# Performance work log

Hardware: AMD Instinct MI355X
Metric: run time of the kernel (lower is better)

The kernel has to match this reference:

```python
import jax, jax.numpy as jnp
import numpy as np

K = 4        # num_kernels
TOPK = 16    # per-row hyperedge sparsification
CHEB_T = 2   # Chebyshev order
ROW_TEMP = 1.0
PI_ITERS = 5  # power-iteration steps


def setup_inputs() -> dict:
    key = jax.random.key(0)
    N, D, D_out = 4096, 256, 256
    ks = jax.random.split(key, 5)
    X = jax.random.normal(ks[0], (N, D), jnp.float32)
    L_k = jax.random.normal(ks[1], (K, D, D), jnp.float32) * 0.02
    alpha = jnp.ones((K,), jnp.float32)
    theta = jax.random.normal(ks[2], (CHEB_T + 1, D), jnp.float32) * 0.02
    rho_raw = jnp.zeros((), jnp.float32)
    proj_w = jax.random.normal(ks[3], (D_out, D), jnp.float32) / np.sqrt(D).astype(np.float32)
    proj_b = jnp.zeros((D_out,), jnp.float32)
    return {"X": X, "L_k": L_k, "alpha": alpha, "theta": theta,
            "rho_raw": rho_raw, "proj_w": proj_w, "proj_b": proj_b}


def reference(X, L_k, alpha, theta, rho_raw, proj_w, proj_b):
    N, D = X.shape
    tau = max(ROW_TEMP, 1e-6)
    # 1) K bilinear kernels: A_k = X L_k X^T / sqrt(D), row-softmax with temp
    A = jnp.einsum('nd,kde,me->knm', X, L_k, X) / jnp.sqrt(jnp.asarray(D, X.dtype))
    H_stack = jax.nn.softmax(A / tau, axis=2)                 # (K, N, N)
    w = jax.nn.softmax(alpha)[:, None, None]
    H_fused = (H_stack * w).sum(0)                            # (N, N)
    # 2) incidence B (N, E=K*N): hyperedge (k,i) holds topk targets of row i of head k
    vals, idx = jax.lax.top_k(H_stack, TOPK)                  # (K, N, TOPK)
    vals = vals / (vals.sum(-1, keepdims=True) + 1e-9)
    E = K * N
    cols = jnp.arange(K)[:, None, None] * N + jnp.arange(N)[None, :, None]
    cols = jnp.broadcast_to(cols, (K, N, TOPK)).reshape(-1)
    rows = idx.reshape(-1)
    B = jnp.zeros((N, E), X.dtype).at[rows, cols].set(vals.reshape(-1))
    W = jnp.ones((E,), X.dtype)
    # 3) normalized hypergraph Laplacian L = I - Dv^{-1/2} B W De^{-1} B^T Dv^{-1/2}
    De = B.sum(0) + 1e-9                                      # (E,)
    Dv = (B * W[None, :]).sum(1) + 1e-9                       # (N,)
    Dv_is = jnp.sqrt(1.0 / Dv)
    S = (B * (W / De)[None, :]) @ B.T                         # (N, N)
    S_norm = Dv_is[:, None] * S * Dv_is[None, :]
    I = jnp.eye(N, dtype=X.dtype)
    L = I - S_norm
    # 4) lambda_max via power iteration on detached L (constant w.r.t. grads)
    Ld = jax.lax.stop_gradient(L)
    v = jax.random.normal(jax.random.key(1), (N, 1), X.dtype)
    v = v / (jnp.linalg.norm(v) + 1e-9)
    for _ in range(PI_ITERS):
        v = Ld @ v
        v = v / (jnp.linalg.norm(v) + 1e-9)
    lam = jnp.clip((v.T @ (Ld @ v)).squeeze(), 1e-3, None)
    lam = jax.lax.stop_gradient(lam)
    L_tilde = (2.0 / lam) * L - I
    # Chebyshev recursion: sum_t T_t(L_tilde) X * theta_t, then ELU
    T0 = X
    out = T0 * theta[0][None, :]
    T1 = L_tilde @ X
    out = out + T1 * theta[1][None, :]
    for t in range(2, CHEB_T + 1):
        T2 = 2.0 * (L_tilde @ T1) - T0
        out = out + T2 * theta[t][None, :]
        T0, T1 = T1, T2
    Z_spec = jax.nn.elu(out)
    # 5) residual blend with kernel diffusion
    Z_kern = H_fused @ X
    rho = jax.nn.sigmoid(rho_raw)
    Z_mix = rho * Z_spec + (1.0 - rho) * Z_kern
    # 6) final projection
    return Z_mix @ proj_w.T + proj_b
```

## Files before the change

### kernel.cpp

```cpp
#include <hip/hip_runtime.h>

typedef unsigned short u16;
typedef unsigned long long u64;
typedef _Float16 h16;
typedef __attribute__((ext_vector_type(8))) _Float16 h16x8;
typedef __attribute__((ext_vector_type(4))) _Float16 h16x4;
typedef __attribute__((ext_vector_type(4))) float f32x4;

__device__ __forceinline__ float b2f(u16 u) {
  unsigned x = ((unsigned)u) << 16;
  return __uint_as_float(x);
}
__device__ __forceinline__ unsigned fkey(float f) {
  unsigned b = __float_as_uint(f);
  return (b & 0x80000000u) ? ~b : (b | 0x80000000u);
}
__device__ __forceinline__ float unfkey(unsigned u) {
  unsigned b = (u & 0x80000000u) ? (u ^ 0x80000000u) : ~u;
  return __uint_as_float(b);
}
__device__ __forceinline__ f32x4 mfma16(h16x8 a, h16x8 b, f32x4 c) {
  return __builtin_amdgcn_mfma_f32_16x16x32_f16(a, b, c, 0, 0, 0);
}
__device__ __forceinline__ void gl_lds16(const void* g, void* l) {
  __builtin_amdgcn_global_load_lds(
      (const __attribute__((address_space(1))) unsigned*)g,
      (__attribute__((address_space(3))) unsigned*)l, 16, 0, 0);
}
__device__ __forceinline__ u64 wave_max_u64(u64 k) {
#pragma unroll
  for (int off = 32; off; off >>= 1) {
    u64 o = __shfl_xor(k, off);
    if (o > k) k = o;
  }
  return k;
}

__global__ void detect_dtype(const u16* __restrict__ X, int* __restrict__ flag) {
  __shared__ int cnt;
  if (threadIdx.x == 0) cnt = 0;
  __syncthreads();
  int sane = 0;
#pragma unroll
  for (int j = 0; j < 16; ++j) {
    u16 u = X[(threadIdx.x * 16 + j) * 2];
    int e = (u >> 7) & 0xff;
    if (u == 0 || (e >= 112 && e <= 142)) sane++;
  }
  atomicAdd(&cnt, sane);
  __syncthreads();
  if (threadIdx.x == 0) *flag = (cnt < 3072) ? 1 : 0;
}

__global__ __launch_bounds__(256) void split_input3(
    const void* __restrict__ in, h16* __restrict__ hi, h16* __restrict__ lo,
    float* __restrict__ f32out, int n, const int* __restrict__ flag) {
  int f = *flag;
  int stride = gridDim.x * 256;
  for (int i = blockIdx.x * 256 + threadIdx.x; i < n; i += stride) {
    float x = f ? ((const float*)in)[i] : b2f(((const u16*)in)[i]);
    h16 h = (h16)x;
    hi[i] = h;
    lo[i] = (h16)(x - (float)h);
    if (f32out) f32out[i] = x;
  }
}

__global__ __launch_bounds__(256) void split_f32h(
    const float* __restrict__ in, h16* __restrict__ hi, h16* __restrict__ lo,
    int n) {
  int stride = gridDim.x * 256;
  for (int i = blockIdx.x * 256 + threadIdx.x; i < n; i += stride) {
    float x = in[i];
    h16 h = (h16)x;
    hi[i] = h;
    lo[i] = (h16)(x - (float)h);
  }
}

__global__ __launch_bounds__(256) void conv_f32(const void* __restrict__ in,
                                                float* __restrict__ out, int n,
                                                const int* __restrict__ flag) {
  int f = *flag;
  int stride = gridDim.x * 256;
  for (int i = blockIdx.x * 256 + threadIdx.x; i < n; i += stride)
    out[i] = f ? ((const float*)in)[i] : b2f(((const u16*)in)[i]);
}

template <bool BIAS>
__global__ __launch_bounds__(256) void gemm3_nt(
    const h16* __restrict__ Ah, const h16* __restrict__ Al,
    const h16* __restrict__ Bh, const h16* __restrict__ Bl,
    float* __restrict__ C, const float* __restrict__ bias, float alpha,
    int M, int Nc, int Kd, long batchA, long batchB, long batchC) {
  const h16* Abh = Ah + (size_t)blockIdx.z * batchA;
  const h16* Abl = Al + (size_t)blockIdx.z * batchA;
  const h16* Bbh = Bh + (size_t)blockIdx.z * batchB;
  const h16* Bbl = Bl + (size_t)blockIdx.z * batchB;
  float* Cb = C + (size_t)blockIdx.z * batchC;
  int bn = blockIdx.x, bm = blockIdx.y;
  int tid = threadIdx.x;
  int wid = tid >> 6, lane = tid & 63;
  __shared__ h16 Ash[64 * 40], Asl[64 * 40], Bsh[64 * 40], Bsl[64 * 40];
  f32x4 acc00 = {}, acc01 = {}, acc10 = {}, acc11 = {};
  int lr = tid >> 2;
  int lc = (tid & 3) << 3;
  size_t aoff = (size_t)(bm * 64 + lr) * Kd + lc;
  size_t boff = (size_t)(bn * 64 + lr) * Kd + lc;
  int wm = (wid & 1) * 32, wn = (wid >> 1) * 32;
  int fr = lane & 15;
  int fc = (lane >> 4) << 3;
  for (int k0 = 0; k0 < Kd; k0 += 32) {
    uint4 avh = *(const uint4*)(Abh + aoff + k0);
    uint4 avl = *(const uint4*)(Abl + aoff + k0);
    uint4 bvh = *(const uint4*)(Bbh + boff + k0);
    uint4 bvl = *(const uint4*)(Bbl + boff + k0);
    __syncthreads();
    *(uint4*)(Ash + lr * 40 + lc) = avh;
    *(uint4*)(Asl + lr * 40 + lc) = avl;
    *(uint4*)(Bsh + lr * 40 + lc) = bvh;
    *(uint4*)(Bsl + lr * 40 + lc) = bvl;
    __syncthreads();
    h16x8 a0h = *(const h16x8*)(Ash + (wm + fr) * 40 + fc);
    h16x8 a1h = *(const h16x8*)(Ash + (wm + 16 + fr) * 40 + fc);
    h16x8 b0h = *(const h16x8*)(Bsh + (wn + fr) * 40 + fc);
    h16x8 b1h = *(const h16x8*)(Bsh + (wn + 16 + fr) * 40 + fc);
    h16x8 a0l = *(const h16x8*)(Asl + (wm + fr) * 40 + fc);
    h16x8 a1l = *(const h16x8*)(Asl + (wm + 16 + fr) * 40 + fc);
    h16x8 b0l = *(const h16x8*)(Bsl + (wn + fr) * 40 + fc);
    h16x8 b1l = *(const h16x8*)(Bsl + (wn + 16 + fr) * 40 + fc);
    acc00 = mfma16(a0h, b0h, acc00);
    acc01 = mfma16(a0h, b1h, acc01);
    acc10 = mfma16(a1h, b0h, acc10);
    acc11 = mfma16(a1h, b1h, acc11);
    acc00 = mfma16(a0h, b0l, acc00);
    acc01 = mfma16(a0h, b1l, acc01);
    acc10 = mfma16(a1h, b0l, acc10);
    acc11 = mfma16(a1h, b1l, acc11);
    acc00 = mfma16(a0l, b0h, acc00);
    acc01 = mfma16(a0l, b1h, acc01);
    acc10 = mfma16(a1l, b0h, acc10);
    acc11 = mfma16(a1l, b1h, acc11);
  }
  int crow = (lane >> 4) << 2;
  int ccol = lane & 15;
  f32x4 accs[2][2] = {{acc00, acc01}, {acc10, acc11}};
#pragma unroll
  for (int i = 0; i < 2; ++i)
#pragma unroll
    for (int j = 0; j < 2; ++j) {
      int r0 = bm * 64 + wm + 16 * i + crow;
      int c0 = bn * 64 + wn + 16 * j + ccol;
#pragma unroll
      for (int rg = 0; rg < 4; ++rg) {
        float v = accs[i][j][rg] * alpha;
        if constexpr (BIAS) v += bias[c0];
        Cb[(size_t)(r0 + rg) * Nc + c0] = v;
      }
    }
}

__global__ __launch_bounds__(256) void gemm3_big(
    const h16* __restrict__ Ah, const h16* __restrict__ Al,
    const h16* __restrict__ Bh, const h16* __restrict__ Bl,
    float* __restrict__ C, float alpha, int M, int Nc, int Kd) {
  __shared__ h16 sAh[128 * 32], sAl[128 * 32], sBh[128 * 32], sBl[128 * 32];
  int tid = threadIdx.x, wid = tid >> 6, lane = tid & 63;
  int bm = blockIdx.y, bn = blockIdx.x;
  int srow = 32 * wid + (lane >> 2);
  int scnk = lane & 3;
  int fr = lane & 15, fcc = lane >> 4;
  f32x4 acc[4][4] = {};
  const h16* gA[2] = {Ah, Al};
  const h16* gB[2] = {Bh, Bl};
  h16* sA[2] = {sAh, sAl};
  h16* sB[2] = {sBh, sBl};
  int wm = (wid & 1) * 64, wn = (wid >> 1) * 64;
  for (int k0 = 0; k0 < Kd; k0 += 32) {
    __syncthreads();
#pragma unroll
    for (int h = 0; h < 2; ++h) {
      int r = srow + 16 * h;
      int cs = scnk ^ ((r >> 1) & 3);
      size_t goffA = (size_t)(bm * 128 + r) * Kd + k0 + cs * 8;
      size_t goffB = (size_t)(bn * 128 + r) * Kd + k0 + cs * 8;
      int loff = (32 * wid + 16 * h) * 32;
#pragma unroll
      for (int p = 0; p < 2; ++p) {
        gl_lds16(gA[p] + goffA, sA[p] + loff);
        gl_lds16(gB[p] + goffB, sB[p] + loff);
      }
    }
    __syncthreads();
    h16x8 fa[2][4], fb[2][4];
#pragma unroll
    for (int i = 0; i < 4; ++i) {
      int ra = wm + 16 * i + fr;
      int ca = (fcc ^ ((ra >> 1) & 3)) * 8;
      fa[0][i] = *(const h16x8*)(sAh + ra * 32 + ca);
      fa[1][i] = *(const h16x8*)(sAl + ra * 32 + ca);
      int rb = wn + 16 * i + fr;
      int cb = (fcc ^ ((rb >> 1) & 3)) * 8;
      fb[0][i] = *(const h16x8*)(sBh + rb * 32 + cb);
      fb[1][i] = *(const h16x8*)(sBl + rb * 32 + cb);
    }
#pragma unroll
    for (int i = 0; i < 4; ++i)
#pragma unroll
      for (int j = 0; j < 4; ++j) {
        acc[i][j] = mfma16(fa[0][i], fb[0][j], acc[i][j]);
        acc[i][j] = mfma16(fa[0][i], fb[1][j], acc[i][j]);
        acc[i][j] = mfma16(fa[1][i], fb[0][j], acc[i][j]);
      }
  }
  int crow = (lane >> 4) << 2, ccol = lane & 15;
#pragma unroll
  for (int i = 0; i < 4; ++i)
#pragma unroll
    for (int j = 0; j < 4; ++j) {
      int r0 = bm * 128 + wm + 16 * i + crow;
      int c0 = bn * 128 + wn + 16 * j + ccol;
#pragma unroll
      for (int rg = 0; rg < 4; ++rg)
        C[(size_t)(r0 + rg) * Nc + c0] = acc[i][j][rg] * alpha;
    }
}

__global__ __launch_bounds__(256) void gemm_ks(
    const h16* __restrict__ A, const h16* __restrict__ B,
    float* __restrict__ Cpart, int Kd, int Kc) {
  __shared__ h16 sA[128 * 32], sB[128 * 32];
  int tid = threadIdx.x, wid = tid >> 6, lane = tid & 63;
  int bm = blockIdx.y, bn = blockIdx.x, kz = blockIdx.z;
  int kbase = kz * Kc;
  int srow = 32 * wid + (lane >> 2);
  int scnk = lane & 3;
  int fr = lane & 15, fcc = lane >> 4;
  f32x4 acc[4][4] = {};
  int wm = (wid & 1) * 64, wn = (wid >> 1) * 64;
  for (int k0 = 0; k0 < Kc; k0 += 32) {
    __syncthreads();
#pragma unroll
    for (int h = 0; h < 2; ++h) {
      int r = srow + 16 * h;
      int cs = scnk ^ ((r >> 1) & 3);
      size_t goffA = (size_t)(bm * 128 + r) * Kd + kbase + k0 + cs * 8;
      size_t goffB = (size_t)(bn * 128 + r) * Kd + kbase + k0 + cs * 8;
      int loff = (32 * wid + 16 * h) * 32;
      gl_lds16(A + goffA, sA + loff);
      gl_lds16(B + goffB, sB + loff);
    }
    __syncthreads();
    h16x8 fa[4], fb[4];
#pragma unroll
    for (int i = 0; i < 4; ++i) {
      int ra = wm + 16 * i + fr;
      int ca = (fcc ^ ((ra >> 1) & 3)) * 8;
      fa[i] = *(const h16x8*)(sA + ra * 32 + ca);
      int rb = wn + 16 * i + fr;
      int cb = (fcc ^ ((rb >> 1) & 3)) * 8;
      fb[i] = *(const h16x8*)(sB + rb * 32 + cb);
    }
#pragma unroll
    for (int i = 0; i < 4; ++i)
#pragma unroll
      for (int j = 0; j < 4; ++j)
        acc[i][j] = mfma16(fa[i], fb[j], acc[i][j]);
  }
  float* Cp = Cpart + (size_t)kz * 4096 * 256;
  int crow = (lane >> 4) << 2, ccol = lane & 15;
#pragma unroll
  for (int i = 0; i < 4; ++i)
#pragma unroll
    for (int j = 0; j < 4; ++j) {
      int r0 = bm * 128 + wm + 16 * i + crow;
      int c0 = bn * 128 + wn + 16 * j + ccol;
#pragma unroll
      for (int rg = 0; rg < 4; ++rg)
        Cp[(size_t)(r0 + rg) * 256 + c0] = acc[i][j][rg];
    }
}

__global__ __launch_bounds__(256) void ks_reduce(
    const float* __restrict__ Cpart, const float* __restrict__ scptr,
    const float* __restrict__ rowSinv, float* __restrict__ Zk) {
  int i = (blockIdx.x * 256 + threadIdx.x) * 4;
  float4 s = {0.f, 0.f, 0.f, 0.f};
#pragma unroll
  for (int z = 0; z < 8; ++z) {
    float4 p = *(const float4*)(Cpart + (size_t)z * 4096 * 256 + i);
    s.x += p.x; s.y += p.y; s.z += p.z; s.w += p.w;
  }
  float sc = (*scptr) * rowSinv[i >> 8];
  float4 zk = *(float4*)(Zk + i);
  zk.x += sc * s.x; zk.y += sc * s.y; zk.z += sc * s.z; zk.w += sc * s.w;
  *(float4*)(Zk + i) = zk;
}

__global__ __launch_bounds__(256) void transpose16(
    const u16* __restrict__ in, u16* __restrict__ out, int rows, int cols) {
  __shared__ u16 t[32][33];
  const u16* ib = in + (size_t)blockIdx.z * rows * cols;
  u16* ob = out + (size_t)blockIdx.z * rows * cols;
  int r0 = blockIdx.x * 32, c0 = blockIdx.y * 32;
  int tx = threadIdx.x & 31, ty = threadIdx.x >> 5;
#pragma unroll
  for (int i = 0; i < 32; i += 8)
    t[ty + i][tx] = ib[(size_t)(r0 + ty + i) * cols + c0 + tx];
  __syncthreads();
#pragma unroll
  for (int i = 0; i < 32; i += 8)
    ob[(size_t)(c0 + ty + i) * rows + r0 + tx] = t[tx][ty + i];
}

__global__ void prep_scalars(const void* __restrict__ alpha,
                             const void* __restrict__ rho_raw,
                             float* __restrict__ scal,
                             const int* __restrict__ flag) {
  if (threadIdx.x == 0) {
    int f = *flag;
    float a[4], e[4], m = -1e30f, s = 0.f;
    for (int i = 0; i < 4; ++i) {
      a[i] = f ? ((const float*)alpha)[i] : b2f(((const u16*)alpha)[i]);
      m = fmaxf(m, a[i]);
    }
    for (int i = 0; i < 4; ++i) { e[i] = expf(a[i] - m); s += e[i]; }
    for (int i = 0; i < 4; ++i) scal[i] = e[i] / s;
    float rr = f ? ((const float*)rho_raw)[0] : b2f(((const u16*)rho_raw)[0]);
    scal[4] = 1.f / (1.f + expf(-rr));
  }
}

__global__ __launch_bounds__(256) void row_softmax_topk(
    const float* __restrict__ A, float* __restrict__ topv,
    int* __restrict__ topi, h16* __restrict__ E, float* __restrict__ rowSinv,
    int khead) {
  __shared__ u64 candK[4][256];
  __shared__ int candN[4];
  int wid = threadIdx.x >> 6, lane = threadIdx.x & 63;
  int row = blockIdx.x * 4 + wid;
  const float* arow = A + ((size_t)row << 12);
  if (lane == 0) candN[wid] = 0;
  __syncthreads();
  float lm = -INFINITY;
#pragma unroll
  for (int t = 0; t < 16; ++t) {
    float4 v = *(const float4*)(arow + (t << 8) + (lane << 2));
    lm = fmaxf(lm, fmaxf(fmaxf(v.x, v.y), fmaxf(v.z, v.w)));
  }
  float m = lm;
#pragma unroll
  for (int off = 32; off; off >>= 1) m = fmaxf(m, __shfl_xor(m, off));
  u64 lk = ((u64)fkey(lm) << 32) | (unsigned)lane;
  float T = 0.f;
  for (int r = 0; r < 16; ++r) {
    u64 k2 = wave_max_u64(lk);
    if (lk == k2) lk = 0;
    if (r == 15) T = unfkey((unsigned)(k2 >> 32));
  }
  h16* erow = E + ((size_t)row << 12);
  int* cn = &candN[wid];
  u64* ck = candK[wid];
  float s = 0.f;
  for (int t = 0; t < 16; ++t) {
    int c = (t << 8) + (lane << 2);
    float4 v = *(const float4*)(arow + c);
    float e0 = __expf(v.x - m), e1 = __expf(v.y - m);
    float e2 = __expf(v.z - m), e3 = __expf(v.w - m);
    s += (e0 + e1) + (e2 + e3);
    h16x4 hv = {(h16)e0, (h16)e1, (h16)e2, (h16)e3};
    *(h16x4*)(erow + c) = hv;
    if (v.x >= T) {
      int sl = atomicAdd(cn, 1);
      if (sl < 256) ck[sl] = ((u64)fkey(v.x) << 32) | (unsigned)(~(unsigned)c);
    }
    if (v.y >= T) {
      int sl = atomicAdd(cn, 1);
      if (sl < 256) ck[sl] = ((u64)fkey(v.y) << 32) | (unsigned)(~(unsigned)(c + 1));
    }
    if (v.z >= T) {
      int sl = atomicAdd(cn, 1);
      if (sl < 256) ck[sl] = ((u64)fkey(v.z) << 32) | (unsigned)(~(unsigned)(c + 2));
    }
    if (v.w >= T) {
      int sl = atomicAdd(cn, 1);
      if (sl < 256) ck[sl] = ((u64)fkey(v.w) << 32) | (unsigned)(~(unsigned)(c + 3));
    }
  }
#pragma unroll
  for (int off = 32; off; off >>= 1) s += __shfl_xor(s, off);
  if (lane == 0) rowSinv[row] = 1.f / s;
  __syncthreads();
  int cnt = min(*cn, 256);
  u64 loc[4] = {0ull, 0ull, 0ull, 0ull};
  int nl = 0;
  for (int j = lane; j < cnt; j += 64)
    if (nl < 4) loc[nl++] = ck[j];
#define CSW(a, b)                     \
  {                                   \
    if (loc[b] > loc[a]) {            \
      u64 tt = loc[a];                \
      loc[a] = loc[b];                \
      loc[b] = tt;                    \
    }                                 \
  }
  CSW(0, 1) CSW(2, 3) CSW(0, 2) CSW(1, 3) CSW(1, 2)
#undef CSW
  float myv = 0.f;
  int myi = 0;
  float sum16 = 0.f;
  for (int r = 0; r < 16; ++r) {
    u64 key = loc[0];
    u64 k2 = wave_max_u64(key);
    float wv = unfkey((unsigned)(k2 >> 32));
    int wi = (int)(~(unsigned)(k2 & 0xffffffffu));
    if (key == k2 && key != 0ull) {
      loc[0] = loc[1];
      loc[1] = loc[2];
      loc[2] = loc[3];
      loc[3] = 0ull;
    }
    sum16 += expf(wv - m);
    if (r == lane) { myv = wv; myi = wi; }
  }
  if (lane < 16) {
    size_t o = (((size_t)khead << 12) + row) * 16 + lane;
    topv[o] = expf(myv - m) / (sum16 + 1e-9f * s);
    topi[o] = myi;
  }
}

__global__ __launch_bounds__(256) void edge_prep2(
    const float* __restrict__ topv, const int* __restrict__ topi,
    float* __restrict__ Dv, int* __restrict__ cnt) {
  int t = blockIdx.x * 256 + threadIdx.x;
  float v = topv[t];
  int i = topi[t];
  atomicAdd(&Dv[i], v);
  atomicAdd(&cnt[i], 1);
}

__global__ __launch_bounds__(256) void edge_deis(
    const float* __restrict__ topv, float* __restrict__ DeIS) {
  int e = blockIdx.x * 256 + threadIdx.x;
  const float4* p = (const float4*)(topv + ((size_t)e << 4));
  float4 a = p[0], b = p[1], c = p[2], d = p[3];
  float s = ((a.x + a.y) + (a.z + a.w)) + ((b.x + b.y) + (b.z + b.w)) +
            ((c.x + c.y) + (c.z + c.w)) + ((d.x + d.y) + (d.z + d.w));
  DeIS[e] = 1.0f / sqrtf(s + 1e-9f);
}

__global__ void dv_isqrt(const float* __restrict__ Dv, float* __restrict__ Dvis) {
  int i = blockIdx.x * 256 + threadIdx.x;
  Dvis[i] = sqrtf(1.0f / (Dv[i] + 1e-9f));
}

__global__ __launch_bounds__(256) void scan_rowptr(const int* __restrict__ cnt,
                                                   int* __restrict__ rowptr,
                                                   int* __restrict__ cur) {
  __shared__ int part[256];
  int tid = threadIdx.x;
  int base = tid * 16;
  int loc[16];
  int s = 0;
#pragma unroll
  for (int j = 0; j < 16; ++j) { loc[j] = s; s += cnt[base + j]; }
  part[tid] = s;
  __syncthreads();
  for (int off = 1; off < 256; off <<= 1) {
    int v = (tid >= off) ? part[tid - off] : 0;
    __syncthreads();
    part[tid] += v;
    __syncthreads();
  }
  int pre = (tid == 0) ? 0 : part[tid - 1];
#pragma unroll
  for (int j = 0; j < 16; ++j) {
    int r = pre + loc[j];
    rowptr[base + j] = r;
    cur[base + j] = r;
  }
  if (tid == 255) rowptr[4096] = part[255];
}

__global__ __launch_bounds__(256) void csr_fill2(
    const float* __restrict__ topv, const int* __restrict__ topi,
    const float* __restrict__ Dvis, const float* __restrict__ DeIS,
    int* __restrict__ cur, float* __restrict__ cvals, int* __restrict__ colE,
    float* __restrict__ cvalR) {
  int t = blockIdx.x * 256 + threadIdx.x;
  int e = t >> 4;
  int i = topi[t];
  float c = Dvis[i] * topv[t] * DeIS[e];
  cvals[t] = c;
  int slot = atomicAdd(&cur[i], 1);
  colE[slot] = e;
  cvalR[slot] = c;
}

__global__ __launch_bounds__(256) void spmv_edge(
    const float* __restrict__ cvals, const int* __restrict__ topi,
    const float* __restrict__ v, float* __restrict__ g) {
  int e = blockIdx.x * 256 + threadIdx.x;
  float acc = 0.f;
#pragma unroll
  for (int p = 0; p < 16; ++p)
    acc += cvals[e * 16 + p] * v[topi[e * 16 + p]];
  g[e] = acc;
}

__global__ __launch_bounds__(256) void spmv_row(
    const int* __restrict__ rowptr, const int* __restrict__ colE,
    const float* __restrict__ cvalR, const float* __restrict__ g,
    const float* __restrict__ vin, float* __restrict__ vout) {
  int wid = threadIdx.x >> 6, lane = threadIdx.x & 63;
  int row = blockIdx.x * 4 + wid;
  int s = rowptr[row], e = rowptr[row + 1];
  float acc = 0.f;
  for (int j = s + lane; j < e; j += 64) acc += cvalR[j] * g[colE[j]];
#pragma unroll
  for (int off = 32; off; off >>= 1) acc += __shfl_xor(acc, off);
  if (lane == 0) vout[row] = vin[row] - acc;
}

__global__ __launch_bounds__(256) void spmm_edge(
    const float* __restrict__ cvals, const int* __restrict__ topi,
    const float* __restrict__ M, float* __restrict__ G) {
  int wid = threadIdx.x >> 6, lane = threadIdx.x & 63;
  int e = blockIdx.x * 4 + wid;
  int cb = lane << 2;
  const float* cv = cvals + ((size_t)e << 4);
  const int* ti = topi + ((size_t)e << 4);
  float cc[16];
  int ix[16];
#pragma unroll
  for (int p = 0; p < 16; ++p) { cc[p] = cv[p]; ix[p] = ti[p]; }
  float4 acc[4] = {};
#pragma unroll
  for (int h = 0; h < 2; ++h) {
    float4 g[8];
#pragma unroll
    for (int p = 0; p < 8; ++p)
      g[p] = *(const float4*)(M + ((size_t)ix[h * 8 + p] << 8) + cb);
#pragma unroll
    for (int p = 0; p < 8; ++p) {
      float c = cc[h * 8 + p];
      float4 gg = g[p];
      int a = p & 3;
      acc[a].x += c * gg.x; acc[a].y += c * gg.y;
      acc[a].z += c * gg.z; acc[a].w += c * gg.w;
    }
  }
  float4 r;
  r.x = (acc[0].x + acc[1].x) + (acc[2].x + acc[3].x);
  r.y = (acc[0].y + acc[1].y) + (acc[2].y + acc[3].y);
  r.z = (acc[0].z + acc[1].z) + (acc[2].z + acc[3].z);
  r.w = (acc[0].w + acc[1].w) + (acc[2].w + acc[3].w);
  *(float4*)(G + ((size_t)e << 8) + cb) = r;
}

__global__ __launch_bounds__(256) void spmm_row(
    const int* __restrict__ rowptr, const int* __restrict__ colE,
    const float* __restrict__ cvalR, const float* __restrict__ G,
    float* __restrict__ Z) {
  int wid = threadIdx.x >> 6, lane = threadIdx.x & 63;
  int row = blockIdx.x * 4 + wid;
  int cb = lane << 2;
  int s = rowptr[row], e = rowptr[row + 1];
  float4 acc[4] = {};
  int j = s;
  for (; j + 8 <= e; j += 8) {
    int ix[8];
    float cc[8];
#pragma unroll
    for (int t = 0; t < 8; ++t) { ix[t] = colE[j + t]; cc[t] = cvalR[j + t]; }
    float4 g[8];
#pragma unroll
    for (int t = 0; t < 8; ++t)
      g[t] = *(const float4*)(G + ((size_t)ix[t] << 8) + cb);
#pragma unroll
    for (int t = 0; t < 8; ++t) {
      float c = cc[t];
      float4 gg = g[t];
      int a = t & 3;
      acc[a].x += c * gg.x; acc[a].y += c * gg.y;
      acc[a].z += c * gg.z; acc[a].w += c * gg.w;
    }
  }
  for (; j < e; ++j) {
    float c = cvalR[j];
    float4 gg = *(const float4*)(G + ((size_t)colE[j] << 8) + cb);
    acc[0].x += c * gg.x; acc[0].y += c * gg.y;
    acc[0].z += c * gg.z; acc[0].w += c * gg.w;
  }
  float4 r;
  r.x = (acc[0].x + acc[1].x) + (acc[2].x + acc[3].x);
  r.y = (acc[0].y + acc[1].y) + (acc[2].y + acc[3].y);
  r.z = (acc[0].z + acc[1].z) + (acc[2].z + acc[3].z);
  r.w = (acc[0].w + acc[1].w) + (acc[2].w + acc[3].w);
  *(float4*)(Z + ((size_t)row << 8) + cb) = r;
}

__global__ __launch_bounds__(256) void init_v0(float* __restrict__ v) {
  int tid = blockIdx.x * 256 + threadIdx.x;
  unsigned j = (unsigned)(tid & 2047);
  unsigned x0 = j, x1 = j + 2048u;
  const unsigned ks0 = 0u, ks1 = 1u, ks2 = 0x1BD11BDAu;
  x0 += ks0; x1 += ks1;
#define TF_R(r)                                  \
  {                                              \
    x0 += x1;                                    \
    x1 = (x1 << (r)) | (x1 >> (32 - (r)));       \
    x1 ^= x0;                                    \
  }
  TF_R(13) TF_R(15) TF_R(26) TF_R(6)  x0 += ks1; x1 += ks2 + 1u;
  TF_R(17) TF_R(29) TF_R(16) TF_R(24) x0 += ks2; x1 += ks0 + 2u;
  TF_R(13) TF_R(15) TF_R(26) TF_R(6)  x0 += ks0; x1 += ks1 + 3u;
  TF_R(17) TF_R(29) TF_R(16) TF_R(24) x0 += ks1; x1 += ks2 + 4u;
  TF_R(13) TF_R(15) TF_R(26) TF_R(6)  x0 += ks2; x1 += ks0 + 5u;
#undef TF_R
  unsigned bits = (tid < 2048) ? x0 : x1;
  float u01 = __uint_as_float((bits >> 9) | 0x3f800000u) - 1.0f;
  const float lo = -0.99999994f;
  float u = fmaxf(lo, u01 * 2.0f + lo);
  float w = -log1pf(-u * u);
  float p;
  if (w < 5.0f) {
    float t = w - 2.5f;
    p = 2.81022636e-08f;
    p = 3.43273939e-07f + p * t;
    p = -3.5233877e-06f + p * t;
    p = -4.39150654e-06f + p * t;
    p = 0.00021858087f + p * t;
    p = -0.00125372503f + p * t;
    p = -0.00417768164f + p * t;
    p = 0.246640727f + p * t;
    p = 1.50140941f + p * t;
  } else {
    float t = sqrtf(w) - 3.0f;
    p = -0.000200214257f;
    p = 0.000100950558f + p * t;
    p = 0.00134934322f + p * t;
    p = -0.00367342844f + p * t;
    p = 0.00573950773f + p * t;
    p = -0.0076224613f + p * t;
    p = 0.00943887047f + p * t;
    p = 1.00167406f + p * t;
    p = 2.83297682f + p * t;
  }
  v[tid] = 1.41421354f * (p * u);
}

__global__ __launch_bounds__(256) void pi_dots(const float* __restrict__ w5,
                                               const float* __restrict__ w6,
                                               float* __restrict__ scal) {
  __shared__ float r1[256], r2[256];
  int tid = threadIdx.x;
  float a = 0.f, b = 0.f;
  for (int i = tid; i < 4096; i += 256) {
    float x = w5[i];
    a += x * x;
    b += x * w6[i];
  }
  r1[tid] = a; r2[tid] = b;
  __syncthreads();
  for (int off = 128; off; off >>= 1) {
    if (tid < off) { r1[tid] += r1[tid + off]; r2[tid] += r2[tid + off]; }
    __syncthreads();
  }
  if (tid == 0) scal[5] = fmaxf(r2[0] / r1[0], 1e-3f);
}

__global__ __launch_bounds__(256) void t1_simple(
    const float* __restrict__ SnX, const float* __restrict__ Xf,
    const float* __restrict__ scal, float* __restrict__ T1) {
  int i = blockIdx.x * 256 + threadIdx.x;
  float c1 = 2.0f / scal[5];
  T1[i] = (c1 - 1.0f) * Xf[i] - c1 * SnX[i];
}

__global__ __launch_bounds__(256) void combine_kernel(
    const float* __restrict__ Xf, const float* __restrict__ T1,
    const float* __restrict__ SnT1, const float* __restrict__ Zk,
    const float* __restrict__ thetaf, const float* __restrict__ scal,
    h16* __restrict__ Zmh, h16* __restrict__ Zml) {
  int idx = blockIdx.x * 256 + threadIdx.x;
  int d = idx & 255;
  float c1 = 2.0f / scal[5];
  float rho = scal[4];
  float x = Xf[idx];
  float t1 = T1[idx];
  float t2 = 2.0f * ((c1 - 1.0f) * t1 - c1 * SnT1[idx]) - x;
  float o = x * thetaf[d] + t1 * thetaf[256 + d] + t2 * thetaf[512 + d];
  float zs = o > 0.0f ? o : expm1f(o);
  float zm = rho * zs + (1.0f - rho) * Zk[idx];
  h16 h = (h16)zm;
  Zmh[idx] = h;
  Zml[idx] = (h16)(zm - (float)h);
}

extern "C" void kernel_launch(void* const* d_in, const int* in_sizes, int n_in,
                              void* d_out, int out_size, void* d_ws,
                              size_t ws_size, hipStream_t stream) {
  (void)in_sizes; (void)n_in; (void)out_size;
  const void* Xin = d_in[0];
  const void* Lin = d_in[1];
  const void* alpha = d_in[2];
  const void* theta = d_in[3];
  const void* rho_raw = d_in[4];
  const void* Wpin = d_in[5];
  const void* bpin = d_in[6];
  float* out = (float*)d_out;

  char* base = (char*)d_ws;
  size_t off = 0;
  auto alloc = [&](size_t bytes) -> char* {
    char* p = base + off;
    off += (bytes + 255) & ~(size_t)255;
    return p;
  };
  float* Abuf = (float*)alloc((size_t)4096 * 4096 * 4);
  h16* Ebuf = (h16*)alloc((size_t)4096 * 4096 * 2);
  h16* Yhi = (h16*)alloc((size_t)4 * 4096 * 256 * 2);
  h16* Ylo = (h16*)alloc((size_t)4 * 4096 * 256 * 2);
  h16* Xhi = (h16*)alloc((size_t)4096 * 256 * 2);
  h16* Xlo = (h16*)alloc((size_t)4096 * 256 * 2);
  float* Xf = (float*)alloc((size_t)4096 * 256 * 4);
  h16* XT = (h16*)alloc((size_t)256 * 4096 * 2);
  h16* Lhi = (h16*)alloc((size_t)4 * 256 * 256 * 2);
  h16* Llo = (h16*)alloc((size_t)4 * 256 * 256 * 2);
  h16* LThi = (h16*)alloc((size_t)4 * 256 * 256 * 2);
  h16* LTlo = (h16*)alloc((size_t)4 * 256 * 256 * 2);
  h16* Whi = (h16*)alloc((size_t)256 * 256 * 2);
  h16* Wlo = (h16*)alloc((size_t)256 * 256 * 2);
  float* Zk = (float*)alloc((size_t)4096 * 256 * 4);
  float* SnX = (float*)alloc((size_t)4096 * 256 * 4);
  float* T1 = (float*)alloc((size_t)4096 * 256 * 4);
  h16* Zmh = (h16*)alloc((size_t)4096 * 256 * 2);
  h16* Zml = (h16*)alloc((size_t)4096 * 256 * 2);
  float* topv = (float*)alloc((size_t)4 * 4096 * 16 * 4);
  int* topi = (int*)alloc((size_t)4 * 4096 * 16 * 4);
  float* cvals = (float*)alloc((size_t)262144 * 4);
  int* colE = (int*)alloc((size_t)262144 * 4);
  float* cvalR = (float*)alloc((size_t)262144 * 4);
  int* rowptr = (int*)alloc(4097 * 4);
  int* cur = (int*)alloc(4096 * 4);
  int* cnt = (int*)alloc(4096 * 4);
  float* Dv = (float*)alloc(4096 * 4);
  float* Dvis = (float*)alloc(4096 * 4);
  float* DeIS = (float*)alloc(16384 * 4);
  float* gE = (float*)alloc(16384 * 4);
  float* wA = (float*)alloc(4096 * 4);
  float* wB = (float*)alloc(4096 * 4);
  float* rowSinv = (float*)alloc(4096 * 4);
  float* thetaf = (float*)alloc(768 * 4);
  float* biasf = (float*)alloc(256 * 4);
  float* scal = (float*)alloc(256);
  int* flag = (int*)alloc(256);
  if (off > ws_size) return;
  float* Yf = (float*)Ebuf;
  float* G = (float*)Abuf;
  float* Kpart = Abuf;

  detect_dtype<<<1, 256, 0, stream>>>((const u16*)Xin, flag);
  split_input3<<<1024, 256, 0, stream>>>(Xin, Xhi, Xlo, Xf, 4096 * 256, flag);
  split_input3<<<256, 256, 0, stream>>>(Lin, Lhi, Llo, nullptr, 4 * 256 * 256,
                                        flag);
  split_input3<<<64, 256, 0, stream>>>(Wpin, Whi, Wlo, nullptr, 256 * 256, flag);
  conv_f32<<<1, 256, 0, stream>>>(theta, thetaf, 768, flag);
  conv_f32<<<1, 256, 0, stream>>>(bpin, biasf, 256, flag);
  prep_scalars<<<1, 64, 0, stream>>>(alpha, rho_raw, scal, flag);
  transpose16<<<dim3(128, 8, 1), 256, 0, stream>>>((const u16*)Xhi, (u16*)XT,
                                                   4096, 256);
  transpose16<<<dim3(8, 8, 4), 256, 0, stream>>>((const u16*)Lhi, (u16*)LThi,
                                                 256, 256);
  transpose16<<<dim3(8, 8, 4), 256, 0, stream>>>((const u16*)Llo, (u16*)LTlo,
                                                 256, 256);
  gemm3_nt<false><<<dim3(4, 64, 4), 256, 0, stream>>>(
      Xhi, Xlo, LThi, LTlo, Yf, nullptr, 1.0f, 4096, 256, 256,
      0L, 256L * 256L, 4096L * 256L);
  split_f32h<<<2048, 256, 0, stream>>>(Yf, Yhi, Ylo, 4 * 4096 * 256);
  hipMemsetAsync(Zk, 0, (size_t)4096 * 256 * 4, stream);
  for (int k = 0; k < 4; ++k) {
    gemm3_big<<<dim3(32, 32), 256, 0, stream>>>(
        Yhi + (size_t)k * 4096 * 256, Ylo + (size_t)k * 4096 * 256, Xhi, Xlo,
        Abuf, 0.0625f, 4096, 4096, 256);
    row_softmax_topk<<<1024, 256, 0, stream>>>(Abuf, topv, topi, Ebuf, rowSinv,
                                               k);
    gemm_ks<<<dim3(2, 32, 8), 256, 0, stream>>>(Ebuf, XT, Kpart, 4096, 512);
    ks_reduce<<<1024, 256, 0, stream>>>(Kpart, scal + k, rowSinv, Zk);
  }
  hipMemsetAsync(Dv, 0, 4096 * 4, stream);
  hipMemsetAsync(cnt, 0, 4096 * 4, stream);
  edge_prep2<<<1024, 256, 0, stream>>>(topv, topi, Dv, cnt);
  edge_deis<<<64, 256, 0, stream>>>(topv, DeIS);
  dv_isqrt<<<16, 256, 0, stream>>>(Dv, Dvis);
  scan_rowptr<<<1, 256, 0, stream>>>(cnt, rowptr, cur);
  csr_fill2<<<1024, 256, 0, stream>>>(topv, topi, Dvis, DeIS, cur, cvals, colE,
                                      cvalR);
  init_v0<<<16, 256, 0, stream>>>(wA);
  for (int it = 0; it < 6; ++it) {
    const float* vi = (it & 1) ? wB : wA;
    float* vo = (it & 1) ? wA : wB;
    spmv_edge<<<64, 256, 0, stream>>>(cvals, topi, vi, gE);
    spmv_row<<<1024, 256, 0, stream>>>(rowptr, colE, cvalR, gE, vi, vo);
  }
  pi_dots<<<1, 256, 0, stream>>>(wB, wA, scal);
  spmm_edge<<<4096, 256, 0, stream>>>(cvals, topi, Xf, G);
  spmm_row<<<1024, 256, 0, stream>>>(rowptr, colE, cvalR, G, SnX);
  t1_simple<<<4096, 256, 0, stream>>>(SnX, Xf, scal, T1);
  spmm_edge<<<4096, 256, 0, stream>>>(cvals, topi, T1, G);
  spmm_row<<<1024, 256, 0, stream>>>(rowptr, colE, cvalR, G, SnX);
  combine_kernel<<<4096, 256, 0, stream>>>(Xf, T1, SnX, Zk, thetaf, scal, Zmh,
                                           Zml);
  gemm3_nt<true><<<dim3(4, 64, 1), 256, 0, stream>>>(
      Zmh, Zml, Whi, Wlo, out, biasf, 1.0f, 4096, 256, 256, 0L, 0L, 0L);
}
```

Before: 761.1 us.

## Build CSR with per-block LDS histograms instead of global atomics

Replaces the global-atomic degree/count histogram with 64 per-block shared-memory histograms, then a column scan that produces per-block base offsets, row counts and Dv^-1/2 in one pass. CSR fill now uses LDS atomics on per-block cursors seeded from rowptr plus the block base, avoiding global atomic contention. It also drops two memsets and the dv_isqrt launch. In exchange it adds about 3 MB of partial buffers and runs the histogram and fill on only 64 blocks.

```diff
diff --git a/kernel.cpp b/kernel.cpp
--- a/kernel.cpp
+++ b/kernel.cpp
@@ -430,14 +430,43 @@
   }
 }
 
-__global__ __launch_bounds__(256) void edge_prep2(
+__global__ __launch_bounds__(256) void hist_part(
     const float* __restrict__ topv, const int* __restrict__ topi,
-    float* __restrict__ Dv, int* __restrict__ cnt) {
-  int t = blockIdx.x * 256 + threadIdx.x;
-  float v = topv[t];
-  int i = topi[t];
-  atomicAdd(&Dv[i], v);
-  atomicAdd(&cnt[i], 1);
+    int* __restrict__ pCnt, float* __restrict__ pDv) {
+  __shared__ int lc[4096];
+  __shared__ float ld[4096];
+  int tid = threadIdx.x, b = blockIdx.x;
+  for (int j = tid; j < 4096; j += 256) { lc[j] = 0; ld[j] = 0.f; }
+  __syncthreads();
+  int base = b * 4096;
+#pragma unroll
+  for (int j = 0; j < 16; ++j) {
+    int t = base + j * 256 + tid;
+    atomicAdd(&lc[topi[t]], 1);
+    atomicAdd(&ld[topi[t]], topv[t]);
+  }
+  __syncthreads();
+  for (int j = tid; j < 4096; j += 256) {
+    pCnt[base + j] = lc[j];
+    pDv[base + j] = ld[j];
+  }
+}
+
+__global__ __launch_bounds__(256) void col_scan(
+    const int* __restrict__ pCnt, const float* __restrict__ pDv,
+    int* __restrict__ cnt, float* __restrict__ Dvis,
+    int* __restrict__ blockBase) {
+  int i = blockIdx.x * 256 + threadIdx.x;
+  int run = 0;
+  float dv = 0.f;
+#pragma unroll
+  for (int b = 0; b < 64; ++b) {
+    blockBase[b * 4096 + i] = run;
+    run += pCnt[b * 4096 + i];
+    dv += pDv[b * 4096 + i];
+  }
+  cnt[i] = run;
+  Dvis[i] = sqrtf(1.0f / (dv + 1e-9f));
 }
 
 __global__ __launch_bounds__(256) void edge_deis(
@@ -450,14 +479,8 @@
   DeIS[e] = 1.0f / sqrtf(s + 1e-9f);
 }
 
-__global__ void dv_isqrt(const float* __restrict__ Dv, float* __restrict__ Dvis) {
-  int i = blockIdx.x * 256 + threadIdx.x;
-  Dvis[i] = sqrtf(1.0f / (Dv[i] + 1e-9f));
-}
-
 __global__ __launch_bounds__(256) void scan_rowptr(const int* __restrict__ cnt,
-                                                   int* __restrict__ rowptr,
-                                                   int* __restrict__ cur) {
+                                                   int* __restrict__ rowptr) {
   __shared__ int part[256];
   int tid = threadIdx.x;
   int base = tid * 16;
@@ -475,27 +498,33 @@
   }
   int pre = (tid == 0) ? 0 : part[tid - 1];
 #pragma unroll
-  for (int j = 0; j < 16; ++j) {
-    int r = pre + loc[j];
-    rowptr[base + j] = r;
-    cur[base + j] = r;
-  }
+  for (int j = 0; j < 16; ++j) rowptr[base + j] = pre + loc[j];
   if (tid == 255) rowptr[4096] = part[255];
 }
 
-__global__ __launch_bounds__(256) void csr_fill2(
+__global__ __launch_bounds__(256) void csr_fill3(
     const float* __restrict__ topv, const int* __restrict__ topi,
     const float* __restrict__ Dvis, const float* __restrict__ DeIS,
-    int* __restrict__ cur, float* __restrict__ cvals, int* __restrict__ colE,
+    const int* __restrict__ rowptr, const int* __restrict__ blockBase,
+    float* __restrict__ cvals, int* __restrict__ colE,
     float* __restrict__ cvalR) {
-  int t = blockIdx.x * 256 + threadIdx.x;
-  int e = t >> 4;
-  int i = topi[t];
-  float c = Dvis[i] * topv[t] * DeIS[e];
-  cvals[t] = c;
-  int slot = atomicAdd(&cur[i], 1);
-  colE[slot] = e;
-  cvalR[slot] = c;
+  __shared__ int lcur[4096];
+  int tid = threadIdx.x, b = blockIdx.x;
+  int base = b * 4096;
+  for (int j = tid; j < 4096; j += 256)
+    lcur[j] = rowptr[j] + blockBase[base + j];
+  __syncthreads();
+#pragma unroll
+  for (int j = 0; j < 16; ++j) {
+    int t = base + j * 256 + tid;
+    int i = topi[t];
+    int e = t >> 4;
+    float c = Dvis[i] * topv[t] * DeIS[e];
+    cvals[t] = c;
+    int slot = atomicAdd(&lcur[i], 1);
+    colE[slot] = e;
+    cvalR[slot] = c;
+  }
 }
 
 __global__ __launch_bounds__(256) void spmv_edge(
@@ -743,10 +772,11 @@
   float* cvals = (float*)alloc((size_t)262144 * 4);
   int* colE = (int*)alloc((size_t)262144 * 4);
   float* cvalR = (float*)alloc((size_t)262144 * 4);
+  int* pCnt = (int*)alloc((size_t)64 * 4096 * 4);
+  float* pDv = (float*)alloc((size_t)64 * 4096 * 4);
+  int* blockBase = (int*)alloc((size_t)64 * 4096 * 4);
   int* rowptr = (int*)alloc(4097 * 4);
-  int* cur = (int*)alloc(4096 * 4);
   int* cnt = (int*)alloc(4096 * 4);
-  float* Dv = (float*)alloc(4096 * 4);
   float* Dvis = (float*)alloc(4096 * 4);
   float* DeIS = (float*)alloc(16384 * 4);
   float* gE = (float*)alloc(16384 * 4);
@@ -790,14 +820,12 @@
     gemm_ks<<<dim3(2, 32, 8), 256, 0, stream>>>(Ebuf, XT, Kpart, 4096, 512);
     ks_reduce<<<1024, 256, 0, stream>>>(Kpart, scal + k, rowSinv, Zk);
   }
-  hipMemsetAsync(Dv, 0, 4096 * 4, stream);
-  hipMemsetAsync(cnt, 0, 4096 * 4, stream);
-  edge_prep2<<<1024, 256, 0, stream>>>(topv, topi, Dv, cnt);
+  hist_part<<<64, 256, 0, stream>>>(topv, topi, pCnt, pDv);
+  col_scan<<<16, 256, 0, stream>>>(pCnt, pDv, cnt, Dvis, blockBase);
   edge_deis<<<64, 256, 0, stream>>>(topv, DeIS);
-  dv_isqrt<<<16, 256, 0, stream>>>(Dv, Dvis);
-  scan_rowptr<<<1, 256, 0, stream>>>(cnt, rowptr, cur);
-  csr_fill2<<<1024, 256, 0, stream>>>(topv, topi, Dvis, DeIS, cur, cvals, colE,
-                                      cvalR);
+  scan_rowptr<<<1, 256, 0, stream>>>(cnt, rowptr);
+  csr_fill3<<<64, 256, 0, stream>>>(topv, topi, Dvis, DeIS, rowptr, blockBase,
+                                    cvals, colE, cvalR);
   init_v0<<<16, 256, 0, stream>>>(wA);
   for (int it = 0; it < 6; ++it) {
     const float* vi = (it & 1) ? wB : wA;
```

Result: faster. 717.9 us (-5.7%).
